# Optimization experiments

Hardware: AMD Instinct MI355X
Metric: run time of the kernel (lower is better)

Reference implementation:

```python
import jax, jax.numpy as jnp
import numpy as np

B, Q, T, H, V = 8, 1, 2048, 512, 32000


def setup_inputs() -> dict:
    key = jax.random.key(0)
    k0, k1, k2, k3, k4 = jax.random.split(key, 5)
    s1 = 1.0 / np.sqrt(2 * H)
    return {
        "input_embeds": jax.random.normal(k0, (B, Q, H), dtype=jnp.float32),
        "target_embeds": jax.random.normal(k1, (B, T, H), dtype=jnp.float32),
        "input_mask": jnp.ones((B, T), dtype=jnp.float32),
        # MLP params: l1 Linear(2H->H, bias), l2 Linear(H->1, no bias)
        "w1": (jax.random.normal(k2, (H, 2 * H), dtype=jnp.float32) * s1),
        "b1": jnp.zeros((H,), dtype=jnp.float32),
        "w2": (jax.random.normal(k3, (H,), dtype=jnp.float32) * (1.0 / np.sqrt(H))),
        # decoder: Linear(H->V, no bias) -> weight [V, H]
        "decoder_weight": (jax.random.normal(k4, (V, H), dtype=jnp.float32) * 0.02),
    }


def reference(input_embeds, target_embeds, input_mask, w1, b1, w2, decoder_weight):
    h = w1.shape[0]
    # l1(cat(q, t)) == q @ W1q^T + t @ W1t^T + b1  (split first linear)
    w1q, w1t = w1[:, :h], w1[:, h:]
    q_proj = jnp.einsum('bqh,kh->bqk', input_embeds, w1q)        # [B,Q,H]
    t_proj = jnp.einsum('bth,kh->btk', target_embeds, w1t)       # [B,T,H]
    # pairwise query x target MLP scoring
    ht = jax.nn.relu(q_proj[:, :, None, :] + t_proj[:, None, :, :] + b1)  # [B,Q,T,H]
    repair_logits = jnp.einsum('bqtk,k->bqt', ht, w2)             # [B,Q,T]
    # _mask: mask*logits - 1000*(1-mask); mask [B,T] -> [B,1,T]
    mask = input_mask[:, None, :]
    repair_logits = mask * repair_logits - 1000.0 * (1.0 - mask)
    # decoder branch: query x vocab-row MLP scoring
    d_proj = jnp.einsum('vh,kh->vk', decoder_weight, w1t)         # [V,H]
    hd = jax.nn.relu(q_proj[:, :, None, :] + d_proj[None, None, :, :] + b1)  # [B,Q,V,H]
    decoder_logits = jnp.einsum('bqvk,k->bqv', hd, w2)            # [B,Q,V]
    out = jnp.concatenate([decoder_logits, repair_logits], axis=2)  # [B,Q,V+T]
    return jnp.squeeze(out, axis=1)  # Q == 1 -> [B, V+T]
```

## Files before the change

kernel.cpp:

```cpp
#include <hip/hip_runtime.h>
#include <hip/hip_bf16.h>

#define Hdim 512
#define Bdim 8
#define Tdim 2048
#define Vdim 32000
#define OUTW (Vdim + Tdim)
#define DEC_TILES (Vdim / 128)
#define REP_TILES ((Bdim * Tdim) / 128)
#define NTILES (DEC_TILES + REP_TILES)

typedef __attribute__((ext_vector_type(8))) short short8;
typedef __attribute__((ext_vector_type(16))) float f32x16;

__device__ __forceinline__ unsigned packbf2(float a, float b) {
    __hip_bfloat162 h = __float22bfloat162_rn(make_float2(a, b));
    union { __hip_bfloat162 h; unsigned u; } c; c.h = h;
    return c.u;
}

union U8 { unsigned u[4]; short8 s; };
__device__ __forceinline__ short8 cvt8(const float4 f0, const float4 f1) {
    U8 r;
    r.u[0] = packbf2(f0.x, f0.y); r.u[1] = packbf2(f0.z, f0.w);
    r.u[2] = packbf2(f1.x, f1.y); r.u[3] = packbf2(f1.z, f1.w);
    return r.s;
}

#define WT_BLOCKS 128
#define QP_BLOCKS (Bdim * Hdim / 4)

__global__ __launch_bounds__(256) void prep_kernel(
    const float* __restrict__ w1, const float* __restrict__ x,
    const float* __restrict__ b1,
    unsigned short* __restrict__ wt, float* __restrict__ qp)
{
    const int bid = blockIdx.x;
    if (bid < WT_BLOCKS) {
        const int i = bid * 256 + threadIdx.x;
        const int n = i >> 6;
        const int kk = (i & 63) * 8;
        const float4* s = (const float4*)(w1 + (size_t)n * 1024 + 512 + kk);
        const float4 v0 = s[0], v1 = s[1];
        uint4 o;
        o.x = packbf2(v0.x, v0.y); o.y = packbf2(v0.z, v0.w);
        o.z = packbf2(v1.x, v1.y); o.w = packbf2(v1.z, v1.w);
        ((uint4*)wt)[i] = o;
    } else {
        const int widx = (bid - WT_BLOCKS) * 4 + (threadIdx.x >> 6);
        const int lane = threadIdx.x & 63;
        const int b = widx >> 9, k = widx & 511;
        const float4* xr = (const float4*)(x + b * Hdim);
        const float4* wr = (const float4*)(w1 + (size_t)k * 1024);
        float4 x0 = xr[lane * 2], x1 = xr[lane * 2 + 1];
        float4 w0 = wr[lane * 2], w1v = wr[lane * 2 + 1];
        float s = x0.x * w0.x + x0.y * w0.y + x0.z * w0.z + x0.w * w0.w
                + x1.x * w1v.x + x1.y * w1v.y + x1.z * w1v.z + x1.w * w1v.w;
#pragma unroll
        for (int off = 32; off > 0; off >>= 1) s += __shfl_down(s, off);
        if (lane == 0) qp[b * Hdim + k] = s + b1[k];
    }
}

__global__ __launch_bounds__(256, 3) void gemm_kernel(
    const float* __restrict__ Adec,
    const float* __restrict__ Atgt,
    const unsigned short* __restrict__ Wt,
    const float* __restrict__ qp,
    const float* __restrict__ w2,
    float* __restrict__ Pd,
    float* __restrict__ Pr)
{
    __shared__ union {
        struct { float A[2][64][64]; unsigned short W[2][64][64]; } g;
        struct { float qT[8][128]; float w2c[128]; } e;
    } u;

    const int tid  = threadIdx.x;
    const int lane = tid & 63;
    const int w    = tid >> 6;

    const int b = blockIdx.x;
    const int mt = (b >> 5) * 8 + (b & 7);
    if (mt >= NTILES) return;
    const int chunk = (b >> 3) & 3;
    const int n0 = chunk << 7;
    const bool is_dec = (mt < DEC_TILES);
    const int m0 = (is_dec ? mt : mt - DEC_TILES) << 7;
    const float* __restrict__ Af = is_dec ? Adec : Atgt;

    const float* gAp[4];
#pragma unroll
    for (int j = 0; j < 4; ++j) {
        const int rr = w * 16 + j * 4 + (lane >> 4);
        const int lc = (lane & 15) ^ (rr & 15);
        gAp[j] = Af + (size_t)(m0 + rr + 64 * (lc >> 3)) * 512 + (lc & 7) * 4;
    }
    const unsigned short* gWp[2];
    {
        const int lcw = (lane & 7) ^ (lane >> 3);
#pragma unroll
        for (int j = 0; j < 2; ++j) {
            const int rr = w * 16 + j * 8 + (lane >> 3);
            gWp[j] = Wt + (size_t)(n0 + rr + 64 * (lcw >> 2)) * 512 + (lcw & 3) * 8;
        }
    }

#define STAGE(bb, koff) do {                                                  \
        _Pragma("unroll")                                                     \
        for (int j = 0; j < 4; ++j)                                           \
            __builtin_amdgcn_global_load_lds(                                 \
                (const __attribute__((address_space(1))) unsigned int*)(gAp[j] + (koff)), \
                (__attribute__((address_space(3))) unsigned int*)(&u.g.A[bb][w * 16 + j * 4][0]), \
                16, 0, 0);                                                    \
        _Pragma("unroll")                                                     \
        for (int j = 0; j < 2; ++j)                                           \
            __builtin_amdgcn_global_load_lds(                                 \
                (const __attribute__((address_space(1))) unsigned int*)(gWp[j] + (koff)), \
                (__attribute__((address_space(3))) unsigned int*)(&u.g.W[bb][w * 16 + j * 8][0]), \
                16, 0, 0);                                                    \
    } while (0)

    f32x16 acc00, acc01, acc10, acc11;
#pragma unroll
    for (int i = 0; i < 16; ++i) { acc00[i] = 0.f; acc01[i] = 0.f; acc10[i] = 0.f; acc11[i] = 0.f; }

    const int wm  = (w & 1) << 6;
    const int wn  = (w >> 1) << 6;
    const int l31 = lane & 31;
    const int kh  = lane >> 5;
    const int rx15 = l31 & 15;
    const int rx7  = l31 & 7;
    const int ha  = wm >> 6;
    const int hw  = wn >> 6;

    STAGE(0, 0);
    __syncthreads();

    int cur = 0;
    for (int t = 0; t < 16; ++t) {
        if (t < 15) STAGE(cur ^ 1, (t + 1) * 32);
        const float (* __restrict__ Ab)[64] = u.g.A[cur];
        const unsigned short (* __restrict__ Wb)[64] = u.g.W[cur];
#pragma unroll
        for (int s = 0; s < 2; ++s) {
            const int g  = s * 2 + kh;
            const int p0 = ((ha * 8 + 2 * g) ^ rx15) << 2;
            const int p1 = ((ha * 8 + 2 * g + 1) ^ rx15) << 2;
            const float4 a0f0 = *(const float4*)&Ab[l31][p0];
            const float4 a0f1 = *(const float4*)&Ab[l31][p1];
            const float4 a1f0 = *(const float4*)&Ab[l31 + 32][p0];
            const float4 a1f1 = *(const float4*)&Ab[l31 + 32][p1];
            const short8 a0 = cvt8(a0f0, a0f1);
            const short8 a1 = cvt8(a1f0, a1f1);
            const int ow = ((hw * 4 + g) ^ rx7) << 3;
            const short8 b0 = *(const short8*)&Wb[l31][ow];
            const short8 b1 = *(const short8*)&Wb[l31 + 32][ow];
            acc00 = __builtin_amdgcn_mfma_f32_32x32x16_bf16(b0, a0, acc00, 0, 0, 0);
            acc01 = __builtin_amdgcn_mfma_f32_32x32x16_bf16(b0, a1, acc01, 0, 0, 0);
            acc10 = __builtin_amdgcn_mfma_f32_32x32x16_bf16(b1, a0, acc10, 0, 0, 0);
            acc11 = __builtin_amdgcn_mfma_f32_32x32x16_bf16(b1, a1, acc11, 0, 0, 0);
        }
        __syncthreads();
        cur ^= 1;
    }
#undef STAGE

    {
        const int qb = tid >> 5;
        const int qn = (tid & 31) << 2;
        *(float4*)&u.e.qT[qb][qn] = *(const float4*)&qp[qb * Hdim + n0 + qn];
        if (tid < 32) *(float4*)&u.e.w2c[tid << 2] = *(const float4*)&w2[n0 + (tid << 2)];
    }
    __syncthreads();

    const int kh4 = kh << 2;
    const int slice = (chunk << 1) + (wn >> 6);

    float4 wvA[4], wvB[4];
#pragma unroll
    for (int run = 0; run < 4; ++run) {
        wvA[run] = *(const float4*)&u.e.w2c[wn + run * 8 + kh4];
        wvB[run] = *(const float4*)&u.e.w2c[wn + 32 + run * 8 + kh4];
    }

#define EPI_PAIR(QROW, T0, T1) do {                                          \
        float _p0 = 0.f, _p1 = 0.f;                                          \
        _Pragma("unroll")                                                    \
        for (int run = 0; run < 4; ++run) {                                  \
            const float4 q0 = *(const float4*)((QROW) + wn + run * 8 + kh4); \
            const float4 q1 = *(const float4*)((QROW) + wn + 32 + run * 8 + kh4); \
            const float4 wA = wvA[run], wB = wvB[run];                       \
            _p0 += fmaxf(acc00[run * 4 + 0] + q0.x, 0.f) * wA.x;             \
            _p1 += fmaxf(acc01[run * 4 + 0] + q0.x, 0.f) * wA.x;             \
            _p0 += fmaxf(acc10[run * 4 + 0] + q1.x, 0.f) * wB.x;             \
            _p1 += fmaxf(acc11[run * 4 + 0] + q1.x, 0.f) * wB.x;             \
            _p0 += fmaxf(acc00[run * 4 + 1] + q0.y, 0.f) * wA.y;             \
            _p1 += fmaxf(acc01[run * 4 + 1] + q0.y, 0.f) * wA.y;             \
            _p0 += fmaxf(acc10[run * 4 + 1] + q1.y, 0.f) * wB.y;             \
            _p1 += fmaxf(acc11[run * 4 + 1] + q1.y, 0.f) * wB.y;             \
            _p0 += fmaxf(acc00[run * 4 + 2] + q0.z, 0.f) * wA.z;             \
            _p1 += fmaxf(acc01[run * 4 + 2] + q0.z, 0.f) * wA.z;             \
            _p0 += fmaxf(acc10[run * 4 + 2] + q1.z, 0.f) * wB.z;             \
            _p1 += fmaxf(acc11[run * 4 + 2] + q1.z, 0.f) * wB.z;             \
            _p0 += fmaxf(acc00[run * 4 + 3] + q0.w, 0.f) * wA.w;             \
            _p1 += fmaxf(acc01[run * 4 + 3] + q0.w, 0.f) * wA.w;             \
            _p0 += fmaxf(acc10[run * 4 + 3] + q1.w, 0.f) * wB.w;             \
            _p1 += fmaxf(acc11[run * 4 + 3] + q1.w, 0.f) * wB.w;             \
        }                                                                    \
        T0 = _p0 + __shfl_xor(_p0, 32);                                      \
        T1 = _p1 + __shfl_xor(_p1, 32);                                      \
    } while (0)

    if (is_dec) {
#pragma unroll
        for (int b2 = 0; b2 < 8; ++b2) {
            float t0, t1;
            EPI_PAIR(&u.e.qT[b2][0], t0, t1);
            if (kh == 0) {
                float* o = Pd + ((size_t)slice * 8 + b2) * Vdim + m0 + wm;
                o[l31]      = t0;
                o[32 + l31] = t1;
            }
        }
    } else {
        const int bfix = m0 >> 11;
        float t0, t1;
        EPI_PAIR(&u.e.qT[bfix][0], t0, t1);
        if (kh == 0) {
            float* o = Pr + (size_t)slice * (Bdim * Tdim) + m0 + wm;
            o[l31]      = t0;
            o[32 + l31] = t1;
        }
    }
#undef EPI_PAIR
}

#define RED_DEC_BLOCKS (Bdim * Vdim / 4 / 256)
#define RED_REP_BLOCKS (Bdim * Tdim / 4 / 256)

__global__ __launch_bounds__(256) void reduce_kernel(
    const float* __restrict__ Pd, const float* __restrict__ Pr,
    const float* __restrict__ mask, float* __restrict__ out)
{
    const int blk = blockIdx.x;
    if (blk < RED_DEC_BLOCKS) {
        const int i4 = blk * 256 + threadIdx.x;
        const int b  = i4 / (Vdim / 4);
        const int v4 = i4 - b * (Vdim / 4);
        const float4* p = (const float4*)Pd + (size_t)b * (Vdim / 4) + v4;
        const size_t cs = (size_t)Bdim * (Vdim / 4);
        float4 s = p[0];
#pragma unroll
        for (int c = 1; c < 8; ++c) {
            const float4 v = p[c * cs];
            s.x += v.x; s.y += v.y; s.z += v.z; s.w += v.w;
        }
        *(float4*)(out + (size_t)b * OUTW + v4 * 4) = s;
    } else {
        const int i4 = (blk - RED_DEC_BLOCKS) * 256 + threadIdx.x;
        const int rr = i4 * 4;
        const int b  = rr >> 11;
        const int t  = rr & 2047;
        const float4* p = (const float4*)Pr + i4;
        const size_t cs = (size_t)(Bdim * Tdim / 4);
        float4 s = p[0];
#pragma unroll
        for (int c = 1; c < 8; ++c) {
            const float4 v = p[c * cs];
            s.x += v.x; s.y += v.y; s.z += v.z; s.w += v.w;
        }
        const float4 mv = *(const float4*)(mask + b * Tdim + t);
        float4 o;
        o.x = mv.x * s.x - 1000.f * (1.f - mv.x);
        o.y = mv.y * s.y - 1000.f * (1.f - mv.y);
        o.z = mv.z * s.z - 1000.f * (1.f - mv.z);
        o.w = mv.w * s.w - 1000.f * (1.f - mv.w);
        *(float4*)(out + (size_t)b * OUTW + Vdim + t) = o;
    }
}

extern "C" void kernel_launch(void* const* d_in, const int* in_sizes, int n_in,
                              void* d_out, int out_size, void* d_ws, size_t ws_size,
                              hipStream_t stream) {
    const float* input_embeds  = (const float*)d_in[0];
    const float* target_embeds = (const float*)d_in[1];
    const float* input_mask    = (const float*)d_in[2];
    const float* w1            = (const float*)d_in[3];
    const float* b1            = (const float*)d_in[4];
    const float* w2            = (const float*)d_in[5];
    const float* decoder_w     = (const float*)d_in[6];
    float* out = (float*)d_out;

    float* qp = (float*)d_ws;
    unsigned short* wt = (unsigned short*)((char*)d_ws + 16384);
    float* Pd = (float*)((char*)d_ws + 16384 + 524288);
    float* Pr = Pd + (size_t)8 * Bdim * Vdim;

    prep_kernel<<<WT_BLOCKS + QP_BLOCKS, 256, 0, stream>>>(w1, input_embeds, b1, wt, qp);
    gemm_kernel<<<48 * 32, 256, 0, stream>>>(
        decoder_w, target_embeds, wt, qp, w2, Pd, Pr);
    reduce_kernel<<<RED_DEC_BLOCKS + RED_REP_BLOCKS, 256, 0, stream>>>(
        Pd, Pr, input_mask, out);
}
```

Baseline: 176.2 us.

## Restructure GEMM K-loop with explicit vmcnt waits and manual double-buffer pipelining

Replaces the __syncthreads-based double-buffer loop with an unrolled two-stage loop. It uses explicit s_waitcnt vmcnt/lgkmcnt, raw s_barrier and sched_barrier fences, so the next tile's global-to-LDS loads stay in flight while the current tile is computed. The aim is to stop __syncthreads from draining all outstanding memory ops on every iteration. The partial vmcnt counts are hand-tuned, so a wrong count could cause a race on the LDS buffers.

```diff
diff --git a/kernel.cpp b/kernel.cpp
--- a/kernel.cpp
+++ b/kernel.cpp
@@ -134,37 +134,56 @@
     const int ha  = wm >> 6;
     const int hw  = wn >> 6;
 
+#define COMPUTE(bb) do {                                                      \
+        _Pragma("unroll")                                                     \
+        for (int s = 0; s < 2; ++s) {                                         \
+            const int g  = s * 2 + kh;                                        \
+            const int p0 = ((ha * 8 + 2 * g) ^ rx15) << 2;                    \
+            const int p1 = ((ha * 8 + 2 * g + 1) ^ rx15) << 2;                \
+            const float4 a0f0 = *(const float4*)&u.g.A[bb][l31][p0];          \
+            const float4 a0f1 = *(const float4*)&u.g.A[bb][l31][p1];          \
+            const float4 a1f0 = *(const float4*)&u.g.A[bb][l31 + 32][p0];     \
+            const float4 a1f1 = *(const float4*)&u.g.A[bb][l31 + 32][p1];     \
+            const short8 a0 = cvt8(a0f0, a0f1);                               \
+            const short8 a1 = cvt8(a1f0, a1f1);                               \
+            const int ow = ((hw * 4 + g) ^ rx7) << 3;                         \
+            const short8 b0 = *(const short8*)&u.g.W[bb][l31][ow];            \
+            const short8 b1 = *(const short8*)&u.g.W[bb][l31 + 32][ow];       \
+            acc00 = __builtin_amdgcn_mfma_f32_32x32x16_bf16(b0, a0, acc00, 0, 0, 0); \
+            acc01 = __builtin_amdgcn_mfma_f32_32x32x16_bf16(b0, a1, acc01, 0, 0, 0); \
+            acc10 = __builtin_amdgcn_mfma_f32_32x32x16_bf16(b1, a0, acc10, 0, 0, 0); \
+            acc11 = __builtin_amdgcn_mfma_f32_32x32x16_bf16(b1, a1, acc11, 0, 0, 0); \
+        }                                                                     \
+    } while (0)
+
+#define SFENCE() __builtin_amdgcn_sched_barrier(0)
+#define WAITL()  do { asm volatile("s_waitcnt lgkmcnt(0)" ::: "memory"); SFENCE(); } while (0)
+#define WAITV(n) do { SFENCE(); asm volatile("s_waitcnt vmcnt(" #n ")" ::: "memory"); SFENCE(); } while (0)
+#define BARRIER() do { __builtin_amdgcn_s_barrier(); SFENCE(); } while (0)
+
     STAGE(0, 0);
-    __syncthreads();
-
-    int cur = 0;
-    for (int t = 0; t < 16; ++t) {
-        if (t < 15) STAGE(cur ^ 1, (t + 1) * 32);
-        const float (* __restrict__ Ab)[64] = u.g.A[cur];
-        const unsigned short (* __restrict__ Wb)[64] = u.g.W[cur];
-#pragma unroll
-        for (int s = 0; s < 2; ++s) {
-            const int g  = s * 2 + kh;
-            const int p0 = ((ha * 8 + 2 * g) ^ rx15) << 2;
-            const int p1 = ((ha * 8 + 2 * g + 1) ^ rx15) << 2;
-            const float4 a0f0 = *(const float4*)&Ab[l31][p0];
-            const float4 a0f1 = *(const float4*)&Ab[l31][p1];
-            const float4 a1f0 = *(const float4*)&Ab[l31 + 32][p0];
-            const float4 a1f1 = *(const float4*)&Ab[l31 + 32][p1];
-            const short8 a0 = cvt8(a0f0, a0f1);
-            const short8 a1 = cvt8(a1f0, a1f1);
-            const int ow = ((hw * 4 + g) ^ rx7) << 3;
-            const short8 b0 = *(const short8*)&Wb[l31][ow];
-            const short8 b1 = *(const short8*)&Wb[l31 + 32][ow];
-            acc00 = __builtin_amdgcn_mfma_f32_32x32x16_bf16(b0, a0, acc00, 0, 0, 0);
-            acc01 = __builtin_amdgcn_mfma_f32_32x32x16_bf16(b0, a1, acc01, 0, 0, 0);
-            acc10 = __builtin_amdgcn_mfma_f32_32x32x16_bf16(b1, a0, acc10, 0, 0, 0);
-            acc11 = __builtin_amdgcn_mfma_f32_32x32x16_bf16(b1, a1, acc11, 0, 0, 0);
-        }
-        __syncthreads();
-        cur ^= 1;
-    }
+    STAGE(1, 32);
+    WAITV(6);
+    BARRIER();
+
+    for (int t = 0; t < 16; t += 2) {
+        COMPUTE(0);
+        WAITL(); BARRIER();
+        if (t < 14) { STAGE(0, (t + 2) * 32); WAITV(6); }
+        else        { WAITV(0); }
+        BARRIER();
+
+        COMPUTE(1);
+        WAITL(); BARRIER();
+        if (t < 14) { STAGE(1, (t + 3) * 32); WAITV(6); BARRIER(); }
+    }
+
+#undef COMPUTE
 #undef STAGE
+#undef WAITL
+#undef WAITV
+#undef BARRIER
+#undef SFENCE
 
     {
         const int qb = tid >> 5;
```

Result: slower. 195.2 us (+10.8%).

## Replace partial-sum buffers and reduce kernel with atomic accumulation into output

Applied to the files above, without the earlier changes.

The GEMM epilogue now atomically adds each slice's partial score directly into the final output instead of writing eight partial slices to workspace. The prep kernel gains extra blocks that initialise the output, zeros for decoder columns and the mask penalty term for repair columns. The mask multiply moves into the GEMM epilogue, and the separate reduce kernel is removed. This saves one kernel launch and the partial-sum write and read traffic. In exchange it adds float atomics with contention across the eight slices per element, and the summation order becomes nondeterministic.

```diff
diff --git a/kernel.cpp b/kernel.cpp
--- a/kernel.cpp
+++ b/kernel.cpp
@@ -29,11 +29,13 @@
 
 #define WT_BLOCKS 128
 #define QP_BLOCKS (Bdim * Hdim / 4)
+#define INIT_BLOCKS (Bdim * OUTW / 4 / 256)
 
 __global__ __launch_bounds__(256) void prep_kernel(
     const float* __restrict__ w1, const float* __restrict__ x,
-    const float* __restrict__ b1,
-    unsigned short* __restrict__ wt, float* __restrict__ qp)
+    const float* __restrict__ b1, const float* __restrict__ mask,
+    unsigned short* __restrict__ wt, float* __restrict__ qp,
+    float* __restrict__ out)
 {
     const int bid = blockIdx.x;
     if (bid < WT_BLOCKS) {
@@ -46,7 +48,7 @@
         o.x = packbf2(v0.x, v0.y); o.y = packbf2(v0.z, v0.w);
         o.z = packbf2(v1.x, v1.y); o.w = packbf2(v1.z, v1.w);
         ((uint4*)wt)[i] = o;
-    } else {
+    } else if (bid < WT_BLOCKS + QP_BLOCKS) {
         const int widx = (bid - WT_BLOCKS) * 4 + (threadIdx.x >> 6);
         const int lane = threadIdx.x & 63;
         const int b = widx >> 9, k = widx & 511;
@@ -59,6 +61,20 @@
 #pragma unroll
         for (int off = 32; off > 0; off >>= 1) s += __shfl_down(s, off);
         if (lane == 0) qp[b * Hdim + k] = s + b1[k];
+    } else {
+        const int idx4 = (bid - WT_BLOCKS - QP_BLOCKS) * 256 + threadIdx.x;
+        const int b = idx4 / (OUTW / 4);
+        const int c4 = (idx4 - b * (OUTW / 4)) * 4;
+        float4 v;
+        if (c4 < Vdim) {
+            v = make_float4(0.f, 0.f, 0.f, 0.f);
+        } else {
+            const int t = c4 - Vdim;
+            const float4 mv = *(const float4*)(mask + b * Tdim + t);
+            v = make_float4(-1000.f * (1.f - mv.x), -1000.f * (1.f - mv.y),
+                            -1000.f * (1.f - mv.z), -1000.f * (1.f - mv.w));
+        }
+        ((float4*)out)[idx4] = v;
     }
 }
 
@@ -68,8 +84,8 @@
     const unsigned short* __restrict__ Wt,
     const float* __restrict__ qp,
     const float* __restrict__ w2,
-    float* __restrict__ Pd,
-    float* __restrict__ Pr)
+    const float* __restrict__ mask,
+    float* __restrict__ out)
 {
     __shared__ union {
         struct { float A[2][64][64]; unsigned short W[2][64][64]; } g;
@@ -175,7 +191,6 @@
     __syncthreads();
 
     const int kh4 = kh << 2;
-    const int slice = (chunk << 1) + (wn >> 6);
 
     float4 wvA[4], wvB[4];
 #pragma unroll
@@ -218,9 +233,9 @@
             float t0, t1;
             EPI_PAIR(&u.e.qT[b2][0], t0, t1);
             if (kh == 0) {
-                float* o = Pd + ((size_t)slice * 8 + b2) * Vdim + m0 + wm;
-                o[l31]      = t0;
-                o[32 + l31] = t1;
+                float* o = out + (size_t)b2 * OUTW + m0 + wm;
+                unsafeAtomicAdd(o + l31, t0);
+                unsafeAtomicAdd(o + 32 + l31, t1);
             }
         }
     } else {
@@ -228,56 +243,16 @@
         float t0, t1;
         EPI_PAIR(&u.e.qT[bfix][0], t0, t1);
         if (kh == 0) {
-            float* o = Pr + (size_t)slice * (Bdim * Tdim) + m0 + wm;
-            o[l31]      = t0;
-            o[32 + l31] = t1;
+            const int t0i = (m0 & 2047) + wm + l31;
+            const int t1i = t0i + 32;
+            const float mv0 = mask[bfix * Tdim + t0i];
+            const float mv1 = mask[bfix * Tdim + t1i];
+            float* o = out + (size_t)bfix * OUTW + Vdim;
+            unsafeAtomicAdd(o + t0i, mv0 * t0);
+            unsafeAtomicAdd(o + t1i, mv1 * t1);
         }
     }
 #undef EPI_PAIR
-}
-
-#define RED_DEC_BLOCKS (Bdim * Vdim / 4 / 256)
-#define RED_REP_BLOCKS (Bdim * Tdim / 4 / 256)
-
-__global__ __launch_bounds__(256) void reduce_kernel(
-    const float* __restrict__ Pd, const float* __restrict__ Pr,
-    const float* __restrict__ mask, float* __restrict__ out)
-{
-    const int blk = blockIdx.x;
-    if (blk < RED_DEC_BLOCKS) {
-        const int i4 = blk * 256 + threadIdx.x;
-        const int b  = i4 / (Vdim / 4);
-        const int v4 = i4 - b * (Vdim / 4);
-        const float4* p = (const float4*)Pd + (size_t)b * (Vdim / 4) + v4;
-        const size_t cs = (size_t)Bdim * (Vdim / 4);
-        float4 s = p[0];
-#pragma unroll
-        for (int c = 1; c < 8; ++c) {
-            const float4 v = p[c * cs];
-            s.x += v.x; s.y += v.y; s.z += v.z; s.w += v.w;
-        }
-        *(float4*)(out + (size_t)b * OUTW + v4 * 4) = s;
-    } else {
-        const int i4 = (blk - RED_DEC_BLOCKS) * 256 + threadIdx.x;
-        const int rr = i4 * 4;
-        const int b  = rr >> 11;
-        const int t  = rr & 2047;
-        const float4* p = (const float4*)Pr + i4;
-        const size_t cs = (size_t)(Bdim * Tdim / 4);
-        float4 s = p[0];
-#pragma unroll
-        for (int c = 1; c < 8; ++c) {
-            const float4 v = p[c * cs];
-            s.x += v.x; s.y += v.y; s.z += v.z; s.w += v.w;
-        }
-        const float4 mv = *(const float4*)(mask + b * Tdim + t);
-        float4 o;
-        o.x = mv.x * s.x - 1000.f * (1.f - mv.x);
-        o.y = mv.y * s.y - 1000.f * (1.f - mv.y);
-        o.z = mv.z * s.z - 1000.f * (1.f - mv.z);
-        o.w = mv.w * s.w - 1000.f * (1.f - mv.w);
-        *(float4*)(out + (size_t)b * OUTW + Vdim + t) = o;
-    }
 }
 
 extern "C" void kernel_launch(void* const* d_in, const int* in_sizes, int n_in,
@@ -294,12 +269,9 @@
 
     float* qp = (float*)d_ws;
     unsigned short* wt = (unsigned short*)((char*)d_ws + 16384);
-    float* Pd = (float*)((char*)d_ws + 16384 + 524288);
-    float* Pr = Pd + (size_t)8 * Bdim * Vdim;
-
-    prep_kernel<<<WT_BLOCKS + QP_BLOCKS, 256, 0, stream>>>(w1, input_embeds, b1, wt, qp);
+
+    prep_kernel<<<WT_BLOCKS + QP_BLOCKS + INIT_BLOCKS, 256, 0, stream>>>(
+        w1, input_embeds, b1, input_mask, wt, qp, out);
     gemm_kernel<<<48 * 32, 256, 0, stream>>>(
-        decoder_w, target_embeds, wt, qp, w2, Pd, Pr);
-    reduce_kernel<<<RED_DEC_BLOCKS + RED_REP_BLOCKS, 256, 0, stream>>>(
-        Pd, Pr, input_mask, out);
-}
+        decoder_w, target_embeds, wt, qp, w2, input_mask, out);
+}
```

Result: no change. 173.2 us, median of 2 (-1.7%).
